# Performance work log

Hardware: AMD Instinct MI355X
Metric: run time of the kernel (lower is better)

Reference implementation:

```python
import jax, jax.numpy as jnp
import numpy as np

N, D, E, EDGE_DIM = 50000, 128, 800000, 3
NEG_SLOPE = 0.2
LN_EPS = 1e-5


def setup_inputs() -> dict:
    key = jax.random.key(0)
    ks = jax.random.split(key, 12)
    s = 1.0 / np.sqrt(D)
    return {
        "x": jax.random.normal(ks[0], (N, D), jnp.float32),
        "edge_index": jax.random.randint(ks[1], (2, E), 0, N, jnp.int32),
        "edge_attr": jax.random.normal(ks[2], (E, EDGE_DIM), jnp.float32),
        "W_l": jax.random.normal(ks[3], (D, D), jnp.float32) * s,
        "b_l": jnp.zeros((D,), jnp.float32),
        "W_r": jax.random.normal(ks[4], (D, D), jnp.float32) * s,
        "b_r": jnp.zeros((D,), jnp.float32),
        "W_e": jax.random.normal(ks[5], (EDGE_DIM, D), jnp.float32) * (1.0 / np.sqrt(EDGE_DIM)),
        "att": jax.random.normal(ks[6], (D,), jnp.float32) * s,
        "bias": jnp.zeros((D,), jnp.float32),
        "res_weight": jnp.array(0.1, jnp.float32),
        "ln_gamma": jnp.ones((D,), jnp.float32),
        "ln_beta": jnp.zeros((D,), jnp.float32),
    }


def reference(x, edge_index, edge_attr, W_l, b_l, W_r, b_r, W_e, att, bias,
              res_weight, ln_gamma, ln_beta):
    src, dst = edge_index[0], edge_index[1]
    # GATv2: lin_l on source, lin_r on target (heads=1, concat=False)
    x_l = x @ W_l + b_l            # [N, D]
    x_r = x @ W_r + b_r            # [N, D]
    e_emb = edge_attr @ W_e        # [E, D]
    # per-edge attention logits
    m = x_l[src] + x_r[dst] + e_emb                      # [E, D]
    m = jnp.where(m > 0, m, NEG_SLOPE * m)               # leaky_relu(0.2)
    alpha = m @ att                                       # [E]
    # segment softmax over destination nodes
    seg_max = jax.ops.segment_max(alpha, dst, num_segments=N)
    seg_max = jnp.where(jnp.isfinite(seg_max), seg_max, 0.0)
    ex = jnp.exp(alpha - seg_max[dst])
    seg_sum = jax.ops.segment_sum(ex, dst, num_segments=N)
    alpha = ex / (seg_sum[dst] + 1e-16)                   # [E]
    # weighted aggregation of transformed source features (dropout off / eval)
    msgs = x_l[src] * alpha[:, None]                      # [E, D]
    out = jax.ops.segment_sum(msgs, dst, num_segments=N) + bias  # [N, D]
    # residual + LayerNorm
    out = x + res_weight * out
    mu = jnp.mean(out, axis=-1, keepdims=True)
    var = jnp.mean(jnp.square(out - mu), axis=-1, keepdims=True)
    out = (out - mu) * jax.lax.rsqrt(var + LN_EPS)
    return out * ln_gamma + ln_beta
```

## Files before the change

kernel.cpp:

```cpp
#include <hip/hip_runtime.h>
#include <hip/hip_bf16.h>

#define N_NODES 50000
#define DIM 128
#define N_EDGES 800000
#define NEG_SLOPE 0.2f
#define LN_EPS 1e-5f
#define SCAN_BS 256
#define NB_SCAN ((N_NODES + SCAN_BS - 1) / SCAN_BS)
#define PADCAP (N_EDGES + 7 * N_NODES)
#define LINPAD 20
#define SCAT_BLOCKS ((N_EDGES + 255) / 256)
#define LIN_BLOCKS  ((N_NODES + 15) / 16)


__device__ __forceinline__ unsigned short f2bf(float f) {
    __hip_bfloat16 h = __float2bfloat16(f);
    return *reinterpret_cast<unsigned short*>(&h);
}

__global__ __launch_bounds__(256) void hist_kernel(const int* __restrict__ dst_idx,
                                                   int* __restrict__ cnt) {
    int i = blockIdx.x * 256 + threadIdx.x;
    int e = i * 4;
    if (e + 4 <= N_EDGES) {
        const int4 d4 = *(const int4*)(dst_idx + e);
        atomicAdd(&cnt[d4.x], 1);
        atomicAdd(&cnt[d4.y], 1);
        atomicAdd(&cnt[d4.z], 1);
        atomicAdd(&cnt[d4.w], 1);
    } else {
        for (; e < N_EDGES; ++e) atomicAdd(&cnt[dst_idx[e]], 1);
    }
}

__global__ __launch_bounds__(SCAN_BS) void scan1_kernel(int* __restrict__ cnt,
                                                        int* __restrict__ partials) {
    __shared__ int sh[SCAN_BS];
    const int i = blockIdx.x * SCAN_BS + threadIdx.x;
    const int deg = (i < N_NODES) ? cnt[i] : 0;
    const int v = (deg + 7) & ~7;
    sh[threadIdx.x] = v;
    __syncthreads();
    for (int off = 1; off < SCAN_BS; off <<= 1) {
        int u = (threadIdx.x >= off) ? sh[threadIdx.x - off] : 0;
        __syncthreads();
        sh[threadIdx.x] += u;
        __syncthreads();
    }
    if (i < N_NODES) cnt[i] = sh[threadIdx.x] - v;
    if (threadIdx.x == SCAN_BS - 1) partials[blockIdx.x] = sh[threadIdx.x];
}

__global__ __launch_bounds__(SCAN_BS) void scan23_kernel(int* __restrict__ cnt,
                                                         const int* __restrict__ partials,
                                                         int* __restrict__ cursor) {
    __shared__ int sh[SCAN_BS];
    const int t = threadIdx.x;
    sh[t] = (t < NB_SCAN) ? partials[t] : 0;
    __syncthreads();
    for (int off = 1; off < SCAN_BS; off <<= 1) {
        int u = (t >= off) ? sh[t - off] : 0;
        __syncthreads();
        sh[t] += u;
        __syncthreads();
    }
    const int boff = (blockIdx.x == 0) ? 0 : sh[blockIdx.x - 1];
    const int i = blockIdx.x * SCAN_BS + t;
    if (i < N_NODES) {
        const int rs = cnt[i] + boff;
        cnt[i] = rs;
        cursor[i] = rs;
    }
}

__global__ __launch_bounds__(256) void lin_scatter_kernel(
    const int* __restrict__ src_idx, const int* __restrict__ dst_idx,
    const float* __restrict__ ea,
    int* __restrict__ cursor, float4* __restrict__ packed,
    const float* __restrict__ x,
    const float* __restrict__ Wl, const float* __restrict__ bl,
    const float* __restrict__ Wr, const float* __restrict__ br,
    __hip_bfloat16* __restrict__ xl_bf, float* __restrict__ xr)
{
    __shared__ float xs[DIM][LINPAD];
    const int t = threadIdx.x;

    if (blockIdx.x < SCAT_BLOCKS) {
        const int e = blockIdx.x * 256 + t;
        if (e >= N_EDGES) return;
        const int pos = atomicAdd(&cursor[dst_idx[e]], 1);
        float4 p;
        p.x = ea[(size_t)e * 3 + 0];
        p.y = ea[(size_t)e * 3 + 1];
        p.z = ea[(size_t)e * 3 + 2];
        p.w = __int_as_float(src_idx[e]);
        packed[pos] = p;
        return;
    }

    const int node0 = (blockIdx.x - SCAT_BLOCKS) * 16;
    for (int idx = t; idx < 16 * DIM; idx += 256) {
        const int n = idx >> 7, k = idx & 127;
        const int gn = node0 + n;
        xs[k][n] = (gn < N_NODES) ? x[(size_t)gn * DIM + k] : 0.f;
    }
    __syncthreads();
    const int tn = (t & 3) * 4;
    const int tc = (t >> 2) * 4;
    const bool is_l = tc < DIM;
    const float* W = is_l ? Wl : Wr;
    const float* b = is_l ? bl : br;
    const int col = is_l ? tc : tc - DIM;
    float4 a0 = {0.f, 0.f, 0.f, 0.f}, a1 = a0, a2 = a0, a3 = a0;
#pragma unroll 4
    for (int k = 0; k < DIM; ++k) {
        const float4 wv = *(const float4*)&W[k * DIM + col];
        const float4 xv = *(const float4*)&xs[k][tn];
        a0.x += xv.x * wv.x; a0.y += xv.x * wv.y; a0.z += xv.x * wv.z; a0.w += xv.x * wv.w;
        a1.x += xv.y * wv.x; a1.y += xv.y * wv.y; a1.z += xv.y * wv.z; a1.w += xv.y * wv.w;
        a2.x += xv.z * wv.x; a2.y += xv.z * wv.y; a2.z += xv.z * wv.z; a2.w += xv.z * wv.w;
        a3.x += xv.w * wv.x; a3.y += xv.w * wv.y; a3.z += xv.w * wv.z; a3.w += xv.w * wv.w;
    }
    const float4 bv = *(const float4*)&b[col];
    a0.x += bv.x; a0.y += bv.y; a0.z += bv.z; a0.w += bv.w;
    a1.x += bv.x; a1.y += bv.y; a1.z += bv.z; a1.w += bv.w;
    a2.x += bv.x; a2.y += bv.y; a2.z += bv.z; a2.w += bv.w;
    a3.x += bv.x; a3.y += bv.y; a3.z += bv.z; a3.w += bv.w;
    float4 acc[4] = {a0, a1, a2, a3};
#pragma unroll
    for (int i = 0; i < 4; ++i) {
        const int gn = node0 + tn + i;
        if (gn >= N_NODES) continue;
        if (is_l) {
            ushort4 u;
            u.x = f2bf(acc[i].x); u.y = f2bf(acc[i].y);
            u.z = f2bf(acc[i].z); u.w = f2bf(acc[i].w);
            *(ushort4*)&xl_bf[(size_t)gn * DIM + col] = u;
        } else {
            *(float4*)&xr[(size_t)gn * DIM + col] = acc[i];
        }
    }
}

#define LOGIT(PX, K, XL0, XL1)                                               \
    {                                                                        \
        float t0 = (XL0) + xrv.x + (K).x * we0.x + (K).y * we1.x + (K).z * we2.x; \
        float t1 = (XL1) + xrv.y + (K).x * we0.y + (K).y * we1.y + (K).z * we2.y; \
        t0 = t0 > 0.f ? t0 : NEG_SLOPE * t0;                                 \
        t1 = t1 > 0.f ? t1 : NEG_SLOPE * t1;                                 \
        PX = t0 * at.x + t1 * at.y;                                          \
    }

__global__ __launch_bounds__(256) void fused_node_kernel(
    const float* __restrict__ x, const __hip_bfloat16* __restrict__ xl_bf,
    const int* __restrict__ row_start, const int* __restrict__ cursor,
    const float4* __restrict__ packed,
    const float* __restrict__ We, const float* __restrict__ att,
    const float* __restrict__ bias, const float* __restrict__ rw_p,
    const float* __restrict__ gamma, const float* __restrict__ beta,
    float* __restrict__ out)
{
    const int wave = blockIdx.x * 4 + (threadIdx.x >> 6);
    const int lane = threadIdx.x & 63;
    const int v0 = wave * 4;
    if (v0 >= N_NODES) return;
    const int loff = 2 * lane;
    const float2 at  = *(const float2*)&att[loff];
    const float2 we0 = *(const float2*)&We[0 * DIM + loff];
    const float2 we1 = *(const float2*)&We[1 * DIM + loff];
    const float2 we2 = *(const float2*)&We[2 * DIM + loff];
    const float2 bi  = *(const float2*)&bias[loff];
    const float2 gm  = *(const float2*)&gamma[loff];
    const float2 bt  = *(const float2*)&beta[loff];
    const float rw = rw_p[0];

    for (int j = 0; j < 4; ++j) {
        const int v = v0 + j;
        if (v >= N_NODES) return;
        const int begin = row_start[v];
        const int end   = cursor[v];
        const size_t nb = (size_t)v * DIM + loff;
        const float2 xrv = *(const float2*)&out[nb];

        float m = -3.4e38f, s = 0.f, a0 = 0.f, a1 = 0.f;
        int pos = begin;
        const int full8 = begin + ((end - begin) & ~7);

        for (; pos < full8; pos += 8) {
            const float4 k0 = packed[pos + 0], k1 = packed[pos + 1];
            const float4 k2 = packed[pos + 2], k3 = packed[pos + 3];
            const float4 k4 = packed[pos + 4], k5 = packed[pos + 5];
            const float4 k6 = packed[pos + 6], k7 = packed[pos + 7];
            const unsigned xu0 = *(const unsigned*)&xl_bf[(size_t)__float_as_int(k0.w) * DIM + loff];
            const unsigned xu1 = *(const unsigned*)&xl_bf[(size_t)__float_as_int(k1.w) * DIM + loff];
            const unsigned xu2 = *(const unsigned*)&xl_bf[(size_t)__float_as_int(k2.w) * DIM + loff];
            const unsigned xu3 = *(const unsigned*)&xl_bf[(size_t)__float_as_int(k3.w) * DIM + loff];
            const unsigned xu4 = *(const unsigned*)&xl_bf[(size_t)__float_as_int(k4.w) * DIM + loff];
            const unsigned xu5 = *(const unsigned*)&xl_bf[(size_t)__float_as_int(k5.w) * DIM + loff];
            const unsigned xu6 = *(const unsigned*)&xl_bf[(size_t)__float_as_int(k6.w) * DIM + loff];
            const unsigned xu7 = *(const unsigned*)&xl_bf[(size_t)__float_as_int(k7.w) * DIM + loff];
            const float xl00 = __uint_as_float(xu0 << 16), xl10 = __uint_as_float(xu0 & 0xffff0000u);
            const float xl01 = __uint_as_float(xu1 << 16), xl11 = __uint_as_float(xu1 & 0xffff0000u);
            const float xl02 = __uint_as_float(xu2 << 16), xl12 = __uint_as_float(xu2 & 0xffff0000u);
            const float xl03 = __uint_as_float(xu3 << 16), xl13 = __uint_as_float(xu3 & 0xffff0000u);
            const float xl04 = __uint_as_float(xu4 << 16), xl14 = __uint_as_float(xu4 & 0xffff0000u);
            const float xl05 = __uint_as_float(xu5 << 16), xl15 = __uint_as_float(xu5 & 0xffff0000u);
            const float xl06 = __uint_as_float(xu6 << 16), xl16 = __uint_as_float(xu6 & 0xffff0000u);
            const float xl07 = __uint_as_float(xu7 << 16), xl17 = __uint_as_float(xu7 & 0xffff0000u);

            float P0, P1, P2, P3, P4, P5, P6, P7;
            LOGIT(P0, k0, xl00, xl10)  LOGIT(P1, k1, xl01, xl11)
            LOGIT(P2, k2, xl02, xl12)  LOGIT(P3, k3, xl03, xl13)
            LOGIT(P4, k4, xl04, xl14)  LOGIT(P5, k5, xl05, xl15)
            LOGIT(P6, k6, xl06, xl16)  LOGIT(P7, k7, xl07, xl17)

            const bool b1 = (lane & 1), b2 = (lane & 2), b4 = (lane & 4);
            float A0, A1, A2, A3, B0, B1, G;
            {
                const float q0 = __shfl_xor(P0, 1, 64), q1 = __shfl_xor(P1, 1, 64);
                const float q2 = __shfl_xor(P2, 1, 64), q3 = __shfl_xor(P3, 1, 64);
                const float q4 = __shfl_xor(P4, 1, 64), q5 = __shfl_xor(P5, 1, 64);
                const float q6 = __shfl_xor(P6, 1, 64), q7 = __shfl_xor(P7, 1, 64);
                A0 = b1 ? (P1 + q1) : (P0 + q0);
                A1 = b1 ? (P3 + q3) : (P2 + q2);
                A2 = b1 ? (P5 + q5) : (P4 + q4);
                A3 = b1 ? (P7 + q7) : (P6 + q6);
            }
            {
                const float q0 = __shfl_xor(A0, 2, 64), q1 = __shfl_xor(A1, 2, 64);
                const float q2 = __shfl_xor(A2, 2, 64), q3 = __shfl_xor(A3, 2, 64);
                B0 = b2 ? (A1 + q1) : (A0 + q0);
                B1 = b2 ? (A3 + q3) : (A2 + q2);
            }
            {
                const float q0 = __shfl_xor(B0, 4, 64), q1 = __shfl_xor(B1, 4, 64);
                G = b4 ? (B1 + q1) : (B0 + q0);
            }
            G += __shfl_xor(G, 8, 64);
            G += __shfl_xor(G, 16, 64);
            G += __shfl_xor(G, 32, 64);
            const float p0 = __shfl(G, 0, 64), p1 = __shfl(G, 1, 64);
            const float p2 = __shfl(G, 2, 64), p3 = __shfl(G, 3, 64);
            const float p4 = __shfl(G, 4, 64), p5 = __shfl(G, 5, 64);
            const float p6 = __shfl(G, 6, 64), p7 = __shfl(G, 7, 64);

            const float pm = fmaxf(fmaxf(fmaxf(p0, p1), fmaxf(p2, p3)),
                                   fmaxf(fmaxf(p4, p5), fmaxf(p6, p7)));
            if (pm <= m + 8.f) {
                const float w0 = __expf(p0 - m), w1 = __expf(p1 - m);
                const float w2 = __expf(p2 - m), w3 = __expf(p3 - m);
                const float w4 = __expf(p4 - m), w5 = __expf(p5 - m);
                const float w6 = __expf(p6 - m), w7 = __expf(p7 - m);
                s  += ((w0 + w1) + (w2 + w3)) + ((w4 + w5) + (w6 + w7));
                a0 += (w0 * xl00 + w1 * xl01 + w2 * xl02 + w3 * xl03)
                    + (w4 * xl04 + w5 * xl05 + w6 * xl06 + w7 * xl07);
                a1 += (w0 * xl10 + w1 * xl11 + w2 * xl12 + w3 * xl13)
                    + (w4 * xl14 + w5 * xl15 + w6 * xl16 + w7 * xl17);
            } else {
                const float mn = fmaxf(m, pm);
                const float f  = __expf(m - mn);
                const float w0 = __expf(p0 - mn), w1 = __expf(p1 - mn);
                const float w2 = __expf(p2 - mn), w3 = __expf(p3 - mn);
                const float w4 = __expf(p4 - mn), w5 = __expf(p5 - mn);
                const float w6 = __expf(p6 - mn), w7 = __expf(p7 - mn);
                s  = s  * f + ((w0 + w1) + (w2 + w3)) + ((w4 + w5) + (w6 + w7));
                a0 = a0 * f + (w0 * xl00 + w1 * xl01 + w2 * xl02 + w3 * xl03)
                            + (w4 * xl04 + w5 * xl05 + w6 * xl06 + w7 * xl07);
                a1 = a1 * f + (w0 * xl10 + w1 * xl11 + w2 * xl12 + w3 * xl13)
                            + (w4 * xl14 + w5 * xl15 + w6 * xl16 + w7 * xl17);
                m = mn;
            }
        }

        if (end - pos >= 4) {
            const float4 k0 = packed[pos + 0], k1 = packed[pos + 1];
            const float4 k2 = packed[pos + 2], k3 = packed[pos + 3];
            const unsigned xu0 = *(const unsigned*)&xl_bf[(size_t)__float_as_int(k0.w) * DIM + loff];
            const unsigned xu1 = *(const unsigned*)&xl_bf[(size_t)__float_as_int(k1.w) * DIM + loff];
            const unsigned xu2 = *(const unsigned*)&xl_bf[(size_t)__float_as_int(k2.w) * DIM + loff];
            const unsigned xu3 = *(const unsigned*)&xl_bf[(size_t)__float_as_int(k3.w) * DIM + loff];
            const float xl00 = __uint_as_float(xu0 << 16), xl10 = __uint_as_float(xu0 & 0xffff0000u);
            const float xl01 = __uint_as_float(xu1 << 16), xl11 = __uint_as_float(xu1 & 0xffff0000u);
            const float xl02 = __uint_as_float(xu2 << 16), xl12 = __uint_as_float(xu2 & 0xffff0000u);
            const float xl03 = __uint_as_float(xu3 << 16), xl13 = __uint_as_float(xu3 & 0xffff0000u);
            float P0, P1, P2, P3;
            LOGIT(P0, k0, xl00, xl10)  LOGIT(P1, k1, xl01, xl11)
            LOGIT(P2, k2, xl02, xl12)  LOGIT(P3, k3, xl03, xl13)
            const float tA0 = __shfl_xor(P0, 1, 64), tA1 = __shfl_xor(P1, 1, 64);
            const float tB0 = __shfl_xor(P2, 1, 64), tB1 = __shfl_xor(P3, 1, 64);
            const bool b0 = (lane & 1);
            float A = b0 ? (P1 + tA1) : (P0 + tA0);
            float B = b0 ? (P3 + tB1) : (P2 + tB0);
            const float tA = __shfl_xor(A, 2, 64), tB = __shfl_xor(B, 2, 64);
            float C = (lane & 2) ? (B + tB) : (A + tA);
            C += __shfl_xor(C, 4, 64);
            C += __shfl_xor(C, 8, 64);
            C += __shfl_xor(C, 16, 64);
            C += __shfl_xor(C, 32, 64);
            const float p0 = __shfl(C, 0, 64), p1 = __shfl(C, 1, 64);
            const float p2 = __shfl(C, 2, 64), p3 = __shfl(C, 3, 64);
            const float pm = fmaxf(fmaxf(p0, p1), fmaxf(p2, p3));
            if (pm <= m + 8.f) {
                const float w0 = __expf(p0 - m), w1 = __expf(p1 - m);
                const float w2 = __expf(p2 - m), w3 = __expf(p3 - m);
                s  += (w0 + w1) + (w2 + w3);
                a0 += w0 * xl00 + w1 * xl01 + w2 * xl02 + w3 * xl03;
                a1 += w0 * xl10 + w1 * xl11 + w2 * xl12 + w3 * xl13;
            } else {
                const float mn = fmaxf(m, pm);
                const float f  = __expf(m - mn);
                const float w0 = __expf(p0 - mn), w1 = __expf(p1 - mn);
                const float w2 = __expf(p2 - mn), w3 = __expf(p3 - mn);
                s  = s  * f + (w0 + w1) + (w2 + w3);
                a0 = a0 * f + w0 * xl00 + w1 * xl01 + w2 * xl02 + w3 * xl03;
                a1 = a1 * f + w0 * xl10 + w1 * xl11 + w2 * xl12 + w3 * xl13;
                m = mn;
            }
            pos += 4;
        }

        for (; pos < end; ++pos) {
            const float4 pk = packed[pos];
            const unsigned xu = *(const unsigned*)&xl_bf[(size_t)__float_as_int(pk.w) * DIM + loff];
            const float xl0 = __uint_as_float(xu << 16);
            const float xl1 = __uint_as_float(xu & 0xffff0000u);
            float p;
            LOGIT(p, pk, xl0, xl1)
#pragma unroll
            for (int o = 32; o > 0; o >>= 1) p += __shfl_xor(p, o, 64);
            if (p <= m + 8.f) {
                const float w = __expf(p - m);
                s += w; a0 += w * xl0; a1 += w * xl1;
            } else {
                const float mn = fmaxf(m, p);
                const float f = __expf(m - mn);
                const float w = __expf(p - mn);
                s = s * f + w; a0 = a0 * f + w * xl0; a1 = a1 * f + w * xl1;
                m = mn;
            }
        }

        const float inv = 1.f / (s + 1e-16f);

        const float2 xv = *(const float2*)&x[nb];
        float u0 = xv.x + rw * (a0 * inv + bi.x);
        float u1 = xv.y + rw * (a1 * inv + bi.y);
        float sum = u0 + u1;
#pragma unroll
        for (int o = 32; o > 0; o >>= 1) sum += __shfl_xor(sum, o, 64);
        const float mu = sum * (1.f / DIM);
        const float d0 = u0 - mu, d1 = u1 - mu;
        float q = d0 * d0 + d1 * d1;
#pragma unroll
        for (int o = 32; o > 0; o >>= 1) q += __shfl_xor(q, o, 64);
        const float rstd = rsqrtf(q * (1.f / DIM) + LN_EPS);
        float2 r;
        r.x = d0 * rstd * gm.x + bt.x;
        r.y = d1 * rstd * gm.y + bt.y;
        *(float2*)&out[nb] = r;
    }
}

extern "C" void kernel_launch(void* const* d_in, const int* in_sizes, int n_in,
                              void* d_out, int out_size, void* d_ws, size_t ws_size,
                              hipStream_t stream)
{
    const float* x    = (const float*)d_in[0];
    const int*   ei   = (const int*)d_in[1];
    const float* ea   = (const float*)d_in[2];
    const float* Wl   = (const float*)d_in[3];
    const float* bl   = (const float*)d_in[4];
    const float* Wr   = (const float*)d_in[5];
    const float* br   = (const float*)d_in[6];
    const float* We   = (const float*)d_in[7];
    const float* att  = (const float*)d_in[8];
    const float* bias = (const float*)d_in[9];
    const float* rw   = (const float*)d_in[10];
    const float* gmm  = (const float*)d_in[11];
    const float* bta  = (const float*)d_in[12];
    float* out = (float*)d_out;

    const int* src_idx = ei;
    const int* dst_idx = ei + N_EDGES;

    __hip_bfloat16* xl_bf = (__hip_bfloat16*)d_ws;
    float4* packed    = (float4*)(xl_bf + (size_t)N_NODES * DIM);
    int*   row_start  = (int*)(packed + PADCAP);
    int*   cursor     = row_start + N_NODES;
    int*   partials   = cursor + N_NODES;

    hipMemsetAsync(row_start, 0, (size_t)N_NODES * sizeof(int), stream);
    hist_kernel<<<(N_EDGES / 4 + 255) / 256, 256, 0, stream>>>(dst_idx, row_start);
    scan1_kernel<<<NB_SCAN, SCAN_BS, 0, stream>>>(row_start, partials);
    scan23_kernel<<<NB_SCAN, SCAN_BS, 0, stream>>>(row_start, partials, cursor);
    lin_scatter_kernel<<<SCAT_BLOCKS + LIN_BLOCKS, 256, 0, stream>>>(
        src_idx, dst_idx, ea, cursor, packed,
        x, Wl, bl, Wr, br, xl_bf, out);
    fused_node_kernel<<<(N_NODES + 15) / 16, 256, 0, stream>>>(x, xl_bf, row_start, cursor,
                                                               packed,
                                                               We, att, bias, rw, gmm, bta, out);
}
```

Measured before the change: 342.1 us.

## Split node linear transform between histogram and scatter kernels

Moves the first half of the node-linear GEMM blocks (1563 of 3125) into the histogram kernel and leaves the rest with the edge scatter kernel, so the atomic-bound histogram and scatter phases each overlap with compute work. It also changes the shared-memory x tile from k-major with padding 20 to node-major with padding 129, reading scalars instead of a float4. The cost is a less balanced split that depends on the fixed LIN_SPLIT constant, and possible bank-conflict or broadcast differences in the new LDS layout.

```diff
diff --git a/kernel.cpp b/kernel.cpp
--- a/kernel.cpp
+++ b/kernel.cpp
@@ -9,9 +9,10 @@
 #define SCAN_BS 256
 #define NB_SCAN ((N_NODES + SCAN_BS - 1) / SCAN_BS)
 #define PADCAP (N_EDGES + 7 * N_NODES)
-#define LINPAD 20
-#define SCAT_BLOCKS ((N_EDGES + 255) / 256)
-#define LIN_BLOCKS  ((N_NODES + 15) / 16)
+#define HIST_B ((N_EDGES / 4 + 255) / 256)
+#define SCAT_B ((N_EDGES + 255) / 256)
+#define LIN_B  ((N_NODES + 15) / 16)
+#define LIN_SPLIT 1563
 
 
 __device__ __forceinline__ unsigned short f2bf(float f) {
@@ -19,91 +20,19 @@
     return *reinterpret_cast<unsigned short*>(&h);
 }
 
-__global__ __launch_bounds__(256) void hist_kernel(const int* __restrict__ dst_idx,
-                                                   int* __restrict__ cnt) {
-    int i = blockIdx.x * 256 + threadIdx.x;
-    int e = i * 4;
-    if (e + 4 <= N_EDGES) {
-        const int4 d4 = *(const int4*)(dst_idx + e);
-        atomicAdd(&cnt[d4.x], 1);
-        atomicAdd(&cnt[d4.y], 1);
-        atomicAdd(&cnt[d4.z], 1);
-        atomicAdd(&cnt[d4.w], 1);
-    } else {
-        for (; e < N_EDGES; ++e) atomicAdd(&cnt[dst_idx[e]], 1);
-    }
-}
-
-__global__ __launch_bounds__(SCAN_BS) void scan1_kernel(int* __restrict__ cnt,
-                                                        int* __restrict__ partials) {
-    __shared__ int sh[SCAN_BS];
-    const int i = blockIdx.x * SCAN_BS + threadIdx.x;
-    const int deg = (i < N_NODES) ? cnt[i] : 0;
-    const int v = (deg + 7) & ~7;
-    sh[threadIdx.x] = v;
-    __syncthreads();
-    for (int off = 1; off < SCAN_BS; off <<= 1) {
-        int u = (threadIdx.x >= off) ? sh[threadIdx.x - off] : 0;
-        __syncthreads();
-        sh[threadIdx.x] += u;
-        __syncthreads();
-    }
-    if (i < N_NODES) cnt[i] = sh[threadIdx.x] - v;
-    if (threadIdx.x == SCAN_BS - 1) partials[blockIdx.x] = sh[threadIdx.x];
-}
-
-__global__ __launch_bounds__(SCAN_BS) void scan23_kernel(int* __restrict__ cnt,
-                                                         const int* __restrict__ partials,
-                                                         int* __restrict__ cursor) {
-    __shared__ int sh[SCAN_BS];
-    const int t = threadIdx.x;
-    sh[t] = (t < NB_SCAN) ? partials[t] : 0;
-    __syncthreads();
-    for (int off = 1; off < SCAN_BS; off <<= 1) {
-        int u = (t >= off) ? sh[t - off] : 0;
-        __syncthreads();
-        sh[t] += u;
-        __syncthreads();
-    }
-    const int boff = (blockIdx.x == 0) ? 0 : sh[blockIdx.x - 1];
-    const int i = blockIdx.x * SCAN_BS + t;
-    if (i < N_NODES) {
-        const int rs = cnt[i] + boff;
-        cnt[i] = rs;
-        cursor[i] = rs;
-    }
-}
-
-__global__ __launch_bounds__(256) void lin_scatter_kernel(
-    const int* __restrict__ src_idx, const int* __restrict__ dst_idx,
-    const float* __restrict__ ea,
-    int* __restrict__ cursor, float4* __restrict__ packed,
+__device__ __forceinline__ void lin_body(
+    int lin_id, int t,
     const float* __restrict__ x,
     const float* __restrict__ Wl, const float* __restrict__ bl,
     const float* __restrict__ Wr, const float* __restrict__ br,
-    __hip_bfloat16* __restrict__ xl_bf, float* __restrict__ xr)
+    __hip_bfloat16* __restrict__ xl_bf, float* __restrict__ xr,
+    float (*xs)[DIM + 1])
 {
-    __shared__ float xs[DIM][LINPAD];
-    const int t = threadIdx.x;
-
-    if (blockIdx.x < SCAT_BLOCKS) {
-        const int e = blockIdx.x * 256 + t;
-        if (e >= N_EDGES) return;
-        const int pos = atomicAdd(&cursor[dst_idx[e]], 1);
-        float4 p;
-        p.x = ea[(size_t)e * 3 + 0];
-        p.y = ea[(size_t)e * 3 + 1];
-        p.z = ea[(size_t)e * 3 + 2];
-        p.w = __int_as_float(src_idx[e]);
-        packed[pos] = p;
-        return;
-    }
-
-    const int node0 = (blockIdx.x - SCAT_BLOCKS) * 16;
+    const int node0 = lin_id * 16;
     for (int idx = t; idx < 16 * DIM; idx += 256) {
         const int n = idx >> 7, k = idx & 127;
         const int gn = node0 + n;
-        xs[k][n] = (gn < N_NODES) ? x[(size_t)gn * DIM + k] : 0.f;
+        xs[n][k] = (gn < N_NODES) ? x[(size_t)gn * DIM + k] : 0.f;
     }
     __syncthreads();
     const int tn = (t & 3) * 4;
@@ -116,11 +45,12 @@
 #pragma unroll 4
     for (int k = 0; k < DIM; ++k) {
         const float4 wv = *(const float4*)&W[k * DIM + col];
-        const float4 xv = *(const float4*)&xs[k][tn];
-        a0.x += xv.x * wv.x; a0.y += xv.x * wv.y; a0.z += xv.x * wv.z; a0.w += xv.x * wv.w;
-        a1.x += xv.y * wv.x; a1.y += xv.y * wv.y; a1.z += xv.y * wv.z; a1.w += xv.y * wv.w;
-        a2.x += xv.z * wv.x; a2.y += xv.z * wv.y; a2.z += xv.z * wv.z; a2.w += xv.z * wv.w;
-        a3.x += xv.w * wv.x; a3.y += xv.w * wv.y; a3.z += xv.w * wv.z; a3.w += xv.w * wv.w;
+        const float x0 = xs[tn + 0][k], x1 = xs[tn + 1][k];
+        const float x2 = xs[tn + 2][k], x3 = xs[tn + 3][k];
+        a0.x += x0 * wv.x; a0.y += x0 * wv.y; a0.z += x0 * wv.z; a0.w += x0 * wv.w;
+        a1.x += x1 * wv.x; a1.y += x1 * wv.y; a1.z += x1 * wv.z; a1.w += x1 * wv.w;
+        a2.x += x2 * wv.x; a2.y += x2 * wv.y; a2.z += x2 * wv.z; a2.w += x2 * wv.w;
+        a3.x += x3 * wv.x; a3.y += x3 * wv.y; a3.z += x3 * wv.z; a3.w += x3 * wv.w;
     }
     const float4 bv = *(const float4*)&b[col];
     a0.x += bv.x; a0.y += bv.y; a0.z += bv.z; a0.w += bv.w;
@@ -141,6 +71,97 @@
             *(float4*)&xr[(size_t)gn * DIM + col] = acc[i];
         }
     }
+}
+
+__global__ __launch_bounds__(256) void hist_lin_kernel(
+    const int* __restrict__ dst_idx, int* __restrict__ cnt,
+    const float* __restrict__ x,
+    const float* __restrict__ Wl, const float* __restrict__ bl,
+    const float* __restrict__ Wr, const float* __restrict__ br,
+    __hip_bfloat16* __restrict__ xl_bf, float* __restrict__ xr)
+{
+    __shared__ float xs[16][DIM + 1];
+    if (blockIdx.x < HIST_B) {
+        const int i = blockIdx.x * 256 + threadIdx.x;
+        int e = i * 4;
+        if (e + 4 <= N_EDGES) {
+            const int4 d4 = *(const int4*)(dst_idx + e);
+            atomicAdd(&cnt[d4.x], 1);
+            atomicAdd(&cnt[d4.y], 1);
+            atomicAdd(&cnt[d4.z], 1);
+            atomicAdd(&cnt[d4.w], 1);
+        } else {
+            for (; e < N_EDGES; ++e) atomicAdd(&cnt[dst_idx[e]], 1);
+        }
+        return;
+    }
+    lin_body(blockIdx.x - HIST_B, threadIdx.x, x, Wl, bl, Wr, br, xl_bf, xr, xs);
+}
+
+__global__ __launch_bounds__(SCAN_BS) void scan1_kernel(int* __restrict__ cnt,
+                                                        int* __restrict__ partials) {
+    __shared__ int sh[SCAN_BS];
+    const int i = blockIdx.x * SCAN_BS + threadIdx.x;
+    const int deg = (i < N_NODES) ? cnt[i] : 0;
+    const int v = (deg + 7) & ~7;
+    sh[threadIdx.x] = v;
+    __syncthreads();
+    for (int off = 1; off < SCAN_BS; off <<= 1) {
+        int u = (threadIdx.x >= off) ? sh[threadIdx.x - off] : 0;
+        __syncthreads();
+        sh[threadIdx.x] += u;
+        __syncthreads();
+    }
+    if (i < N_NODES) cnt[i] = sh[threadIdx.x] - v;
+    if (threadIdx.x == SCAN_BS - 1) partials[blockIdx.x] = sh[threadIdx.x];
+}
+
+__global__ __launch_bounds__(SCAN_BS) void scan23_kernel(int* __restrict__ cnt,
+                                                         const int* __restrict__ partials,
+                                                         int* __restrict__ cursor) {
+    __shared__ int sh[SCAN_BS];
+    const int t = threadIdx.x;
+    sh[t] = (t < NB_SCAN) ? partials[t] : 0;
+    __syncthreads();
+    for (int off = 1; off < SCAN_BS; off <<= 1) {
+        int u = (t >= off) ? sh[t - off] : 0;
+        __syncthreads();
+        sh[t] += u;
+        __syncthreads();
+    }
+    const int boff = (blockIdx.x == 0) ? 0 : sh[blockIdx.x - 1];
+    const int i = blockIdx.x * SCAN_BS + t;
+    if (i < N_NODES) {
+        const int rs = cnt[i] + boff;
+        cnt[i] = rs;
+        cursor[i] = rs;
+    }
+}
+
+__global__ __launch_bounds__(256) void scatter_lin_kernel(
+    const int* __restrict__ src_idx, const int* __restrict__ dst_idx,
+    const float* __restrict__ ea,
+    int* __restrict__ cursor, float4* __restrict__ packed,
+    const float* __restrict__ x,
+    const float* __restrict__ Wl, const float* __restrict__ bl,
+    const float* __restrict__ Wr, const float* __restrict__ br,
+    __hip_bfloat16* __restrict__ xl_bf, float* __restrict__ xr)
+{
+    __shared__ float xs[16][DIM + 1];
+    if (blockIdx.x < SCAT_B) {
+        const int e = blockIdx.x * 256 + threadIdx.x;
+        if (e >= N_EDGES) return;
+        const int pos = atomicAdd(&cursor[dst_idx[e]], 1);
+        float4 p;
+        p.x = ea[(size_t)e * 3 + 0];
+        p.y = ea[(size_t)e * 3 + 1];
+        p.z = ea[(size_t)e * 3 + 2];
+        p.w = __int_as_float(src_idx[e]);
+        packed[pos] = p;
+        return;
+    }
+    lin_body(LIN_SPLIT + (blockIdx.x - SCAT_B), threadIdx.x,
+             x, Wl, bl, Wr, br, xl_bf, xr, xs);
 }
 
 #define LOGIT(PX, K, XL0, XL1)                                               \
@@ -391,10 +412,11 @@
     int*   partials   = cursor + N_NODES;
 
     hipMemsetAsync(row_start, 0, (size_t)N_NODES * sizeof(int), stream);
-    hist_kernel<<<(N_EDGES / 4 + 255) / 256, 256, 0, stream>>>(dst_idx, row_start);
+    hist_lin_kernel<<<HIST_B + LIN_SPLIT, 256, 0, stream>>>(
+        dst_idx, row_start, x, Wl, bl, Wr, br, xl_bf, out);
     scan1_kernel<<<NB_SCAN, SCAN_BS, 0, stream>>>(row_start, partials);
     scan23_kernel<<<NB_SCAN, SCAN_BS, 0, stream>>>(row_start, partials, cursor);
-    lin_scatter_kernel<<<SCAT_BLOCKS + LIN_BLOCKS, 256, 0, stream>>>(
+    scatter_lin_kernel<<<SCAT_B + (LIN_B - LIN_SPLIT), 256, 0, stream>>>(
         src_idx, dst_idx, ea, cursor, packed,
         x, Wl, bl, Wr, br, xl_bf, out);
     fused_node_kernel<<<(N_NODES + 15) / 16, 256, 0, stream>>>(x, xl_bf, row_start, cursor,
```

After: 351.4 us. 1.03x slower.
